# Kernel tuning notes

Measured on AMD Instinct MI355X. Metric: run time of the kernel, lower is better.

Reference implementation:

```python
import jax, jax.numpy as jnp
import numpy as np

B, S, EH, DH, A = 32, 2048, 512, 512, 512

def setup_inputs() -> dict:
    key = jax.random.key(0)
    k1, k2, k3, k4, k5 = jax.random.split(key, 5)
    decoder_hidden = jax.random.normal(k1, (2, B, DH), dtype=jnp.float32)
    encoder_outputs = jax.random.normal(k2, (B, S, 2 * EH), dtype=jnp.float32)
    # Linear weights stored as (in, out) for x @ W convention
    W = jax.random.normal(k3, (2 * EH, A), dtype=jnp.float32) / np.sqrt(2 * EH)
    U = jax.random.normal(k4, (2 * DH, A), dtype=jnp.float32) / np.sqrt(2 * DH)
    v = jax.random.normal(k5, (A, 1), dtype=jnp.float32) / np.sqrt(A)
    return {"decoder_hidden": decoder_hidden, "encoder_outputs": encoder_outputs,
            "W": W, "U": U, "v": v}

def reference(decoder_hidden, encoder_outputs, W, U, v):
    # (2, B, DH) -> (B, 2*DH), matching transpose(0,1).reshape(B, -1)
    b = decoder_hidden.shape[1]
    dh = jnp.transpose(decoder_hidden, (1, 0, 2)).reshape(b, -1)
    temp1 = jnp.einsum('bse,ea->bsa', encoder_outputs, W)   # (B, S, A)
    temp2 = dh @ U                                          # (B, A) — computed once, broadcast over S
    score = jnp.squeeze(jnp.tanh(temp1 + temp2[:, None, :]) @ v, -1)  # (B, S)
    attention_weights = jax.nn.softmax(score, axis=-1)      # (B, S)
    context_vector = jnp.einsum('bs,bse->be', attention_weights, encoder_outputs)[:, None, :]  # (B,1,2EH)
    return context_vector, attention_weights
```

## Files before the change

### kernel.cpp

```cpp
#include <hip/hip_runtime.h>
#include <hip/hip_bf16.h>

#define Bb 32
#define Ss 2048
#define Kk 1024
#define Aa 512

#define BM 128
#define BK 64
#define NT (Kk / BK)
#define ABUF (BM * BK * 2)
#define BBUF (Aa * BK * 2)

typedef __bf16 bf16x8 __attribute__((ext_vector_type(8)));
typedef float f32x4 __attribute__((ext_vector_type(4)));

__device__ __forceinline__ unsigned short f2bf(float f) {
  unsigned u = __float_as_uint(f);
  u += 0x7FFFu + ((u >> 16) & 1u);
  return (unsigned short)(u >> 16);
}

__device__ __forceinline__ float tanh_fast(float x) {
  float e = __expf(2.f * x);
  return (e - 1.f) / (e + 1.f);
}

__device__ __forceinline__ void gll16(const void* g, void* l) {
  __builtin_amdgcn_global_load_lds(
      (const __attribute__((address_space(1))) unsigned int*)g,
      (__attribute__((address_space(3))) unsigned int*)l, 16, 0, 0);
}

__global__ __launch_bounds__(256) void prep_wt(const float* __restrict__ W,
                                               unsigned short* __restrict__ WtT) {
  const int idx = blockIdx.x * 256 + threadIdx.x;
  const int a = idx & 511;
  const int g = idx >> 9;
  const int k0 = g * 8;
  const int t = k0 >> 6, kin = k0 & 63;
  unsigned short u[8];
#pragma unroll
  for (int j = 0; j < 8; ++j) u[j] = f2bf(W[(size_t)(k0 + j) * Aa + a]);
  uint4 pk;
  pk.x = (unsigned)u[0] | ((unsigned)u[1] << 16);
  pk.y = (unsigned)u[2] | ((unsigned)u[3] << 16);
  pk.z = (unsigned)u[4] | ((unsigned)u[5] << 16);
  pk.w = (unsigned)u[6] | ((unsigned)u[7] << 16);
  const size_t byteoff = (size_t)t * 65536 + a * 128 + (((kin * 2) ^ ((a & 7) << 4)));
  *(uint4*)((char*)WtT + byteoff) = pk;
}

__global__ __launch_bounds__(256) void t2_partial(const float* __restrict__ dh,
                                                  const float* __restrict__ U,
                                                  float* __restrict__ part) {
  const int b = blockIdx.x, kc = blockIdx.y, t = threadIdx.x;
  __shared__ float sdh[128];
  if (t < 128) {
    int k = kc * 128 + t;
    sdh[t] = dh[(k >> 9) * (Bb * 512) + b * 512 + (k & 511)];
  }
  __syncthreads();
#pragma unroll
  for (int h = 0; h < 2; ++h) {
    const int a = h * 256 + t;
    float s = 0.f;
#pragma unroll 8
    for (int kk = 0; kk < 128; ++kk) s += sdh[kk] * U[(size_t)(kc * 128 + kk) * Aa + a];
    part[(size_t)(b * 8 + kc) * Aa + a] = s;
  }
}

__global__ __launch_bounds__(256) void t2_reduce(const float* __restrict__ part,
                                                 float* __restrict__ t2) {
  const int idx = blockIdx.x * 256 + threadIdx.x;
  const int b = idx >> 9, a = idx & 511;
  float s = 0.f;
#pragma unroll
  for (int kc = 0; kc < 8; ++kc) s += part[(size_t)(b * 8 + kc) * Aa + a];
  t2[idx] = s;
}

#define STEP(curA, curB, nxtA, nxtB, T)                                         \
  {                                                                             \
    const int tn = (T) + 1;                                                     \
    float4 av0, av1, av2, av3;                                                  \
    if (tn < NT) {                                                              \
      const float* eb = encBase + tn * BK;                                      \
      av0 = *(const float4*)(eb + (size_t)(a_r0)      * Kk + a_c);              \
      av1 = *(const float4*)(eb + (size_t)(a_r0 + 32) * Kk + a_c);              \
      av2 = *(const float4*)(eb + (size_t)(a_r0 + 64) * Kk + a_c);              \
      av3 = *(const float4*)(eb + (size_t)(a_r0 + 96) * Kk + a_c);              \
      const char* gB = (const char*)WtT + (size_t)tn * 65536;                   \
      _Pragma("unroll")                                                         \
      for (int q = 0; q < 8; ++q)                                               \
        gll16(gB + (tid + q * 512) * 16, (nxtB) + (tid + q * 512) * 16);        \
    }                                                                           \
    _Pragma("unroll")                                                           \
    for (int kk = 0; kk < 2; ++kk) {                                            \
      bf16x8 af[4], bfr[8];                                                     \
      const int kb = (kk * 32 + ((lane >> 4) << 3)) * 2;                        \
      _Pragma("unroll")                                                         \
      for (int mi = 0; mi < 4; ++mi) {                                          \
        int r = wy * 64 + mi * 16 + (lane & 15);                                \
        af[mi] = *(const bf16x8*)((curA) + r * 128 + (kb ^ ((r & 7) << 4)));    \
      }                                                                         \
      _Pragma("unroll")                                                         \
      for (int ni = 0; ni < 8; ++ni) {                                          \
        int a = wx * 128 + ni * 16 + (lane & 15);                               \
        bfr[ni] = *(const bf16x8*)((curB) + a * 128 + (kb ^ ((a & 7) << 4)));   \
      }                                                                         \
      _Pragma("unroll")                                                         \
      for (int mi = 0; mi < 4; ++mi)                                            \
        _Pragma("unroll")                                                       \
        for (int ni = 0; ni < 8; ++ni)                                          \
          acc[mi][ni] = __builtin_amdgcn_mfma_f32_16x16x32_bf16(af[mi], bfr[ni], acc[mi][ni], 0, 0, 0); \
    }                                                                           \
    if (tn < NT) {                                                              \
      ushort4 w;                                                                \
      w.x = f2bf(av0.x); w.y = f2bf(av0.y); w.z = f2bf(av0.z); w.w = f2bf(av0.w); \
      *(ushort4*)((nxtA) + (a_r0)      * 128 + a_swz) = w;                      \
      w.x = f2bf(av1.x); w.y = f2bf(av1.y); w.z = f2bf(av1.z); w.w = f2bf(av1.w); \
      *(ushort4*)((nxtA) + (a_r0 + 32) * 128 + a_swz) = w;                      \
      w.x = f2bf(av2.x); w.y = f2bf(av2.y); w.z = f2bf(av2.z); w.w = f2bf(av2.w); \
      *(ushort4*)((nxtA) + (a_r0 + 64) * 128 + a_swz) = w;                      \
      w.x = f2bf(av3.x); w.y = f2bf(av3.y); w.z = f2bf(av3.z); w.w = f2bf(av3.w); \
      *(ushort4*)((nxtA) + (a_r0 + 96) * 128 + a_swz) = w;                      \
    }                                                                           \
    __syncthreads();                                                            \
  }

__global__ __launch_bounds__(512, 2) void score_gemm(const float* __restrict__ enc,
                                                     const unsigned short* __restrict__ WtT,
                                                     const float* __restrict__ t2,
                                                     const float* __restrict__ v,
                                                     float* __restrict__ score) {
  __shared__ __align__(16) char lds[2 * (ABUF + BBUF)];
  char* sA0 = lds;
  char* sA1 = lds + ABUF;
  char* sB0 = lds + 2 * ABUF;
  char* sB1 = lds + 2 * ABUF + BBUF;

  const int blk = blockIdx.x;
  const int b = blk >> 4, sc = blk & 15;
  const float* encBase = enc + (size_t)(b * Ss + sc * BM) * Kk;

  const int tid = threadIdx.x;
  const int lane = tid & 63;
  const int wid = tid >> 6;
  const int wy = wid >> 2, wx = wid & 3;

  const int a_r0 = tid >> 4;
  const int a_c = (tid & 15) << 2;
  const int a_swz = (a_c * 2) ^ ((a_r0 & 7) << 4);

  const f32x4 zero = {0.f, 0.f, 0.f, 0.f};
  f32x4 acc[4][8];
#pragma unroll
  for (int i = 0; i < 4; ++i)
#pragma unroll
    for (int j = 0; j < 8; ++j) acc[i][j] = zero;

  {
    float4 av0 = *(const float4*)(encBase + (size_t)(a_r0)      * Kk + a_c);
    float4 av1 = *(const float4*)(encBase + (size_t)(a_r0 + 32) * Kk + a_c);
    float4 av2 = *(const float4*)(encBase + (size_t)(a_r0 + 64) * Kk + a_c);
    float4 av3 = *(const float4*)(encBase + (size_t)(a_r0 + 96) * Kk + a_c);
#pragma unroll
    for (int q = 0; q < 8; ++q)
      gll16((const char*)WtT + (tid + q * 512) * 16, sB0 + (tid + q * 512) * 16);
    ushort4 w;
    w.x = f2bf(av0.x); w.y = f2bf(av0.y); w.z = f2bf(av0.z); w.w = f2bf(av0.w);
    *(ushort4*)(sA0 + (a_r0)      * 128 + a_swz) = w;
    w.x = f2bf(av1.x); w.y = f2bf(av1.y); w.z = f2bf(av1.z); w.w = f2bf(av1.w);
    *(ushort4*)(sA0 + (a_r0 + 32) * 128 + a_swz) = w;
    w.x = f2bf(av2.x); w.y = f2bf(av2.y); w.z = f2bf(av2.z); w.w = f2bf(av2.w);
    *(ushort4*)(sA0 + (a_r0 + 64) * 128 + a_swz) = w;
    w.x = f2bf(av3.x); w.y = f2bf(av3.y); w.z = f2bf(av3.z); w.w = f2bf(av3.w);
    *(ushort4*)(sA0 + (a_r0 + 96) * 128 + a_swz) = w;
    __syncthreads();
  }

  for (int t = 0; t < NT; t += 2) {
    STEP(sA0, sB0, sA1, sB1, t)
    STEP(sA1, sB1, sA0, sB0, t + 1)
  }

  float t2v[8], vv[8];
#pragma unroll
  for (int ni = 0; ni < 8; ++ni) {
    int c = wx * 128 + ni * 16 + (lane & 15);
    t2v[ni] = t2[b * Aa + c];
    vv[ni] = v[c];
  }
  float sp[4][4];
#pragma unroll
  for (int mi = 0; mi < 4; ++mi)
#pragma unroll
    for (int j = 0; j < 4; ++j) sp[mi][j] = 0.f;
#pragma unroll
  for (int mi = 0; mi < 4; ++mi)
#pragma unroll
    for (int ni = 0; ni < 8; ++ni)
#pragma unroll
      for (int j = 0; j < 4; ++j) {
        float x = acc[mi][ni][j] + t2v[ni];
        sp[mi][j] += vv[ni] * tanh_fast(x);
      }

  float* sbuf = (float*)lds;
#pragma unroll
  for (int mi = 0; mi < 4; ++mi)
#pragma unroll
    for (int j = 0; j < 4; ++j) {
      float s = sp[mi][j];
      s += __shfl_xor(s, 1);
      s += __shfl_xor(s, 2);
      s += __shfl_xor(s, 4);
      s += __shfl_xor(s, 8);
      if ((lane & 15) == 0) {
        int r = wy * 64 + mi * 16 + ((lane >> 4) << 2) + j;
        sbuf[r * 4 + wx] = s;
      }
    }
  __syncthreads();
  if (tid < BM) {
    float s = sbuf[tid * 4] + sbuf[tid * 4 + 1] + sbuf[tid * 4 + 2] + sbuf[tid * 4 + 3];
    score[b * Ss + sc * BM + tid] = s;
  }
}

__global__ __launch_bounds__(256) void softmax_k(float* __restrict__ aw) {
  const int b = blockIdx.x, t = threadIdx.x;
  __shared__ float red[8];
  float s[8];
  float m = -3.4e38f;
#pragma unroll
  for (int i = 0; i < 8; ++i) {
    s[i] = aw[b * Ss + t + i * 256];
    m = fmaxf(m, s[i]);
  }
#pragma unroll
  for (int off = 1; off < 64; off <<= 1) m = fmaxf(m, __shfl_xor(m, off));
  const int lane = t & 63, wv = t >> 6;
  if (lane == 0) red[wv] = m;
  __syncthreads();
  m = fmaxf(fmaxf(red[0], red[1]), fmaxf(red[2], red[3]));
  float e[8];
  float l = 0.f;
#pragma unroll
  for (int i = 0; i < 8; ++i) { e[i] = __expf(s[i] - m); l += e[i]; }
#pragma unroll
  for (int off = 1; off < 64; off <<= 1) l += __shfl_xor(l, off);
  if (lane == 0) red[4 + wv] = l;
  __syncthreads();
  l = red[4] + red[5] + red[6] + red[7];
  const float inv = 1.f / l;
#pragma unroll
  for (int i = 0; i < 8; ++i) aw[b * Ss + t + i * 256] = e[i] * inv;
}

__global__ __launch_bounds__(256) void ctx_partial(const float* __restrict__ enc,
                                                   const float* __restrict__ aw,
                                                   float* __restrict__ part) {
  const int b = blockIdx.x, ch = blockIdx.y, t = threadIdx.x;
  __shared__ float sw[64];
  const int s0 = ch * 64;
  if (t < 64) sw[t] = aw[b * Ss + s0 + t];
  __syncthreads();
  float ax = 0.f, ay = 0.f, az = 0.f, aww = 0.f;
  const float* ebase = enc + (size_t)(b * Ss + s0) * Kk + t * 4;
#pragma unroll 4
  for (int r = 0; r < 64; ++r) {
    const float4 ev = *(const float4*)(ebase + (size_t)r * Kk);
    const float w = sw[r];
    ax += w * ev.x; ay += w * ev.y; az += w * ev.z; aww += w * ev.w;
  }
  float4 o; o.x = ax; o.y = ay; o.z = az; o.w = aww;
  *(float4*)(part + (size_t)(b * 32 + ch) * Kk + t * 4) = o;
}

__global__ __launch_bounds__(256) void ctx_reduce(const float* __restrict__ part,
                                                  float* __restrict__ ctx) {
  const int idx = blockIdx.x * 256 + threadIdx.x;
  const int b = idx >> 10, e = idx & 1023;
  float s = 0.f;
#pragma unroll
  for (int ch = 0; ch < 32; ++ch) s += part[(size_t)(b * 32 + ch) * Kk + e];
  ctx[idx] = s;
}

extern "C" void kernel_launch(void* const* d_in, const int* in_sizes, int n_in,
                              void* d_out, int out_size, void* d_ws, size_t ws_size,
                              hipStream_t stream) {
  const float* dh  = (const float*)d_in[0];
  const float* enc = (const float*)d_in[1];
  const float* W   = (const float*)d_in[2];
  const float* U   = (const float*)d_in[3];
  const float* v   = (const float*)d_in[4];

  float* out_ctx = (float*)d_out;
  float* out_aw  = (float*)d_out + 32768;

  char* ws = (char*)d_ws;
  unsigned short* WtT = (unsigned short*)ws;
  float* t2p   = (float*)(ws + 1048576);
  float* t2    = (float*)(ws + 1048576 + 524288);
  float* cpart = (float*)(ws + 1048576 + 524288 + 65536);

  prep_wt<<<256, 256, 0, stream>>>(W, WtT);
  t2_partial<<<dim3(32, 8), 256, 0, stream>>>(dh, U, t2p);
  t2_reduce<<<64, 256, 0, stream>>>(t2p, t2);
  score_gemm<<<512, 512, 0, stream>>>(enc, WtT, t2, v, out_aw);
  softmax_k<<<32, 256, 0, stream>>>(out_aw);
  ctx_partial<<<dim3(32, 32), 256, 0, stream>>>(enc, out_aw, cpart);
  ctx_reduce<<<128, 256, 0, stream>>>(cpart, out_ctx);
}
```

Before: 196.8 us.

## Load fp32 encoder tiles directly to LDS and convert to bf16 at fragment read

The encoder A tile is now staged into LDS as raw fp32 with global_load_lds (direct-to-LDS DMA) and converted to bf16 only when fragments are read, instead of going through registers with a conversion and ds_write. The K step shrinks to 32, W's pre-transposed layout becomes a plain per-K-group layout, and the loop becomes a two-stage async pipeline with explicit vmcnt waits, raw s_barrier and setprio around the MFMA block. The aim is to take register staging and conversion off the load path and overlap global loads with compute. In exchange the A buffer needs twice the LDS per K element, conversion work is repeated by each wave reading the tile, and the occupancy hint of 2 blocks per CU is dropped.

```diff
diff --git a/kernel.cpp b/kernel.cpp
--- a/kernel.cpp
+++ b/kernel.cpp
@@ -7,13 +7,14 @@
 #define Aa 512
 
 #define BM 128
-#define BK 64
+#define BK 32
 #define NT (Kk / BK)
-#define ABUF (BM * BK * 2)
+#define ABUF (BM * BK * 4)
 #define BBUF (Aa * BK * 2)
 
 typedef __bf16 bf16x8 __attribute__((ext_vector_type(8)));
 typedef float f32x4 __attribute__((ext_vector_type(4)));
+typedef float f32x8 __attribute__((ext_vector_type(8)));
 
 __device__ __forceinline__ unsigned short f2bf(float f) {
   unsigned u = __float_as_uint(f);
@@ -36,9 +37,9 @@
                                                unsigned short* __restrict__ WtT) {
   const int idx = blockIdx.x * 256 + threadIdx.x;
   const int a = idx & 511;
-  const int g = idx >> 9;
-  const int k0 = g * 8;
-  const int t = k0 >> 6, kin = k0 & 63;
+  const int o = idx >> 9;
+  const int t = o >> 2, g = o & 3;
+  const int k0 = o * 8;
   unsigned short u[8];
 #pragma unroll
   for (int j = 0; j < 8; ++j) u[j] = f2bf(W[(size_t)(k0 + j) * Aa + a]);
@@ -47,8 +48,7 @@
   pk.y = (unsigned)u[2] | ((unsigned)u[3] << 16);
   pk.z = (unsigned)u[4] | ((unsigned)u[5] << 16);
   pk.w = (unsigned)u[6] | ((unsigned)u[7] << 16);
-  const size_t byteoff = (size_t)t * 65536 + a * 128 + (((kin * 2) ^ ((a & 7) << 4)));
-  *(uint4*)((char*)WtT + byteoff) = pk;
+  *(uint4*)((char*)WtT + (size_t)t * 32768 + g * 8192 + a * 16) = pk;
 }
 
 __global__ __launch_bounds__(256) void t2_partial(const float* __restrict__ dh,
@@ -81,60 +81,56 @@
   t2[idx] = s;
 }
 
-#define STEP(curA, curB, nxtA, nxtB, T)                                         \
+#define ITER(curA, curB, T)                                                     \
   {                                                                             \
-    const int tn = (T) + 1;                                                     \
-    float4 av0, av1, av2, av3;                                                  \
-    if (tn < NT) {                                                              \
-      const float* eb = encBase + tn * BK;                                      \
-      av0 = *(const float4*)(eb + (size_t)(a_r0)      * Kk + a_c);              \
-      av1 = *(const float4*)(eb + (size_t)(a_r0 + 32) * Kk + a_c);              \
-      av2 = *(const float4*)(eb + (size_t)(a_r0 + 64) * Kk + a_c);              \
-      av3 = *(const float4*)(eb + (size_t)(a_r0 + 96) * Kk + a_c);              \
-      const char* gB = (const char*)WtT + (size_t)tn * 65536;                   \
-      _Pragma("unroll")                                                         \
-      for (int q = 0; q < 8; ++q)                                               \
-        gll16(gB + (tid + q * 512) * 16, (nxtB) + (tid + q * 512) * 16);        \
+    bf16x8 af[4], bfr[8];                                                       \
+    _Pragma("unroll")                                                           \
+    for (int mi = 0; mi < 4; ++mi) {                                            \
+      const int r = wy * 64 + mi * 16 + (lane & 15);                            \
+      const int c0 = r * 8 + (((lane >> 4) * 2) ^ ((r & 3) << 1));              \
+      f32x4 lo = *(const f32x4*)((curA) + c0 * 16);                             \
+      f32x4 hi = *(const f32x4*)((curA) + c0 * 16 + 16);                        \
+      f32x8 w8 = {lo.x, lo.y, lo.z, lo.w, hi.x, hi.y, hi.z, hi.w};              \
+      af[mi] = __builtin_convertvector(w8, bf16x8);                             \
     }                                                                           \
     _Pragma("unroll")                                                           \
-    for (int kk = 0; kk < 2; ++kk) {                                            \
-      bf16x8 af[4], bfr[8];                                                     \
-      const int kb = (kk * 32 + ((lane >> 4) << 3)) * 2;                        \
+    for (int ni = 0; ni < 8; ++ni) {                                            \
+      const int a = wx * 128 + ni * 16 + (lane & 15);                           \
+      bfr[ni] = *(const bf16x8*)((curB) + (lane >> 4) * 8192 + a * 16);         \
+    }                                                                           \
+    __builtin_amdgcn_s_setprio(1);                                              \
+    _Pragma("unroll")                                                           \
+    for (int mi = 0; mi < 4; ++mi)                                              \
       _Pragma("unroll")                                                         \
-      for (int mi = 0; mi < 4; ++mi) {                                          \
-        int r = wy * 64 + mi * 16 + (lane & 15);                                \
-        af[mi] = *(const bf16x8*)((curA) + r * 128 + (kb ^ ((r & 7) << 4)));    \
-      }                                                                         \
-      _Pragma("unroll")                                                         \
-      for (int ni = 0; ni < 8; ++ni) {                                          \
-        int a = wx * 128 + ni * 16 + (lane & 15);                               \
-        bfr[ni] = *(const bf16x8*)((curB) + a * 128 + (kb ^ ((a & 7) << 4)));   \
-      }                                                                         \
-      _Pragma("unroll")                                                         \
-      for (int mi = 0; mi < 4; ++mi)                                            \
-        _Pragma("unroll")                                                       \
-        for (int ni = 0; ni < 8; ++ni)                                          \
-          acc[mi][ni] = __builtin_amdgcn_mfma_f32_16x16x32_bf16(af[mi], bfr[ni], acc[mi][ni], 0, 0, 0); \
+      for (int ni = 0; ni < 8; ++ni)                                            \
+        acc[mi][ni] = __builtin_amdgcn_mfma_f32_16x16x32_bf16(af[mi], bfr[ni], acc[mi][ni], 0, 0, 0); \
+    __builtin_amdgcn_s_setprio(0);                                              \
+    __builtin_amdgcn_sched_barrier(0);                                          \
+    __builtin_amdgcn_s_barrier();          \
+    if ((T) + 2 < NT) {                                                         \
+      const char* eb = encB + ((T) + 2) * 128;                                  \
+      gll16(eb + a_goff0, (curA) + a_loff0);                                    \
+      gll16(eb + a_goff1, (curA) + a_loff1);                                    \
+      const char* wb = wtB + (size_t)((T) + 2) * 32768;                         \
+      gll16(wb + b_off0, (curB) + b_off0);                                      \
+      gll16(wb + b_off1, (curB) + b_off1);                                      \
+      gll16(wb + b_off2, (curB) + b_off2);                                      \
+      gll16(wb + b_off3, (curB) + b_off3);                                      \
     }                                                                           \
-    if (tn < NT) {                                                              \
-      ushort4 w;                                                                \
-      w.x = f2bf(av0.x); w.y = f2bf(av0.y); w.z = f2bf(av0.z); w.w = f2bf(av0.w); \
-      *(ushort4*)((nxtA) + (a_r0)      * 128 + a_swz) = w;                      \
-      w.x = f2bf(av1.x); w.y = f2bf(av1.y); w.z = f2bf(av1.z); w.w = f2bf(av1.w); \
-      *(ushort4*)((nxtA) + (a_r0 + 32) * 128 + a_swz) = w;                      \
-      w.x = f2bf(av2.x); w.y = f2bf(av2.y); w.z = f2bf(av2.z); w.w = f2bf(av2.w); \
-      *(ushort4*)((nxtA) + (a_r0 + 64) * 128 + a_swz) = w;                      \
-      w.x = f2bf(av3.x); w.y = f2bf(av3.y); w.z = f2bf(av3.z); w.w = f2bf(av3.w); \
-      *(ushort4*)((nxtA) + (a_r0 + 96) * 128 + a_swz) = w;                      \
+    if ((T) < NT - 2) {                                                         \
+      asm volatile("s_waitcnt vmcnt(6)" ::: "memory");                          \
+    } else {                                                                    \
+      asm volatile("s_waitcnt vmcnt(0)" ::: "memory");                          \
     }                                                                           \
-    __syncthreads();                                                            \
-  }
-
-__global__ __launch_bounds__(512, 2) void score_gemm(const float* __restrict__ enc,
-                                                     const unsigned short* __restrict__ WtT,
-                                                     const float* __restrict__ t2,
-                                                     const float* __restrict__ v,
-                                                     float* __restrict__ score) {
+    __builtin_amdgcn_sched_barrier(0);                                          \
+    __builtin_amdgcn_s_barrier();                         \
+  }
+
+__global__ __launch_bounds__(512) void score_gemm(const float* __restrict__ enc,
+                                                  const unsigned short* __restrict__ WtT,
+                                                  const float* __restrict__ t2,
+                                                  const float* __restrict__ v,
+                                                  float* __restrict__ score) {
   __shared__ __align__(16) char lds[2 * (ABUF + BBUF)];
   char* sA0 = lds;
   char* sA1 = lds + ABUF;
@@ -143,16 +139,26 @@
 
   const int blk = blockIdx.x;
   const int b = blk >> 4, sc = blk & 15;
-  const float* encBase = enc + (size_t)(b * Ss + sc * BM) * Kk;
+  const char* encB = (const char*)(enc + (size_t)(b * Ss + sc * BM) * Kk);
+  const char* wtB = (const char*)WtT;
 
   const int tid = threadIdx.x;
   const int lane = tid & 63;
   const int wid = tid >> 6;
   const int wy = wid >> 2, wx = wid & 3;
 
-  const int a_r0 = tid >> 4;
-  const int a_c = (tid & 15) << 2;
-  const int a_swz = (a_c * 2) ^ ((a_r0 & 7) << 4);
+  const int a_c0 = tid, a_c1 = 512 + tid;
+  const int a_r0 = a_c0 >> 3, a_r1 = a_c1 >> 3;
+  const int a_h0 = (a_c0 & 7) ^ ((a_r0 & 3) << 1);
+  const int a_h1 = (a_c1 & 7) ^ ((a_r1 & 3) << 1);
+  const int a_goff0 = a_r0 * 4096 + a_h0 * 16;
+  const int a_goff1 = a_r1 * 4096 + a_h1 * 16;
+  const int a_loff0 = a_c0 * 16;
+  const int a_loff1 = a_c1 * 16;
+  const int b_off0 = tid * 16;
+  const int b_off1 = (512 + tid) * 16;
+  const int b_off2 = (1024 + tid) * 16;
+  const int b_off3 = (1536 + tid) * 16;
 
   const f32x4 zero = {0.f, 0.f, 0.f, 0.f};
   f32x4 acc[4][8];
@@ -162,28 +168,28 @@
     for (int j = 0; j < 8; ++j) acc[i][j] = zero;
 
   {
-    float4 av0 = *(const float4*)(encBase + (size_t)(a_r0)      * Kk + a_c);
-    float4 av1 = *(const float4*)(encBase + (size_t)(a_r0 + 32) * Kk + a_c);
-    float4 av2 = *(const float4*)(encBase + (size_t)(a_r0 + 64) * Kk + a_c);
-    float4 av3 = *(const float4*)(encBase + (size_t)(a_r0 + 96) * Kk + a_c);
-#pragma unroll
-    for (int q = 0; q < 8; ++q)
-      gll16((const char*)WtT + (tid + q * 512) * 16, sB0 + (tid + q * 512) * 16);
-    ushort4 w;
-    w.x = f2bf(av0.x); w.y = f2bf(av0.y); w.z = f2bf(av0.z); w.w = f2bf(av0.w);
-    *(ushort4*)(sA0 + (a_r0)      * 128 + a_swz) = w;
-    w.x = f2bf(av1.x); w.y = f2bf(av1.y); w.z = f2bf(av1.z); w.w = f2bf(av1.w);
-    *(ushort4*)(sA0 + (a_r0 + 32) * 128 + a_swz) = w;
-    w.x = f2bf(av2.x); w.y = f2bf(av2.y); w.z = f2bf(av2.z); w.w = f2bf(av2.w);
-    *(ushort4*)(sA0 + (a_r0 + 64) * 128 + a_swz) = w;
-    w.x = f2bf(av3.x); w.y = f2bf(av3.y); w.z = f2bf(av3.z); w.w = f2bf(av3.w);
-    *(ushort4*)(sA0 + (a_r0 + 96) * 128 + a_swz) = w;
-    __syncthreads();
+    gll16(encB + a_goff0, sA0 + a_loff0);
+    gll16(encB + a_goff1, sA0 + a_loff1);
+    gll16(wtB + b_off0, sB0 + b_off0);
+    gll16(wtB + b_off1, sB0 + b_off1);
+    gll16(wtB + b_off2, sB0 + b_off2);
+    gll16(wtB + b_off3, sB0 + b_off3);
+    const char* eb1 = encB + 128;
+    gll16(eb1 + a_goff0, sA1 + a_loff0);
+    gll16(eb1 + a_goff1, sA1 + a_loff1);
+    const char* wb1 = wtB + 32768;
+    gll16(wb1 + b_off0, sB1 + b_off0);
+    gll16(wb1 + b_off1, sB1 + b_off1);
+    gll16(wb1 + b_off2, sB1 + b_off2);
+    gll16(wb1 + b_off3, sB1 + b_off3);
+    asm volatile("s_waitcnt vmcnt(6)" ::: "memory");
+    __builtin_amdgcn_sched_barrier(0);
+    __builtin_amdgcn_s_barrier();
   }
 
   for (int t = 0; t < NT; t += 2) {
-    STEP(sA0, sB0, sA1, sB1, t)
-    STEP(sA1, sB1, sA0, sB0, t + 1)
+    ITER(sA0, sB0, t)
+    ITER(sA1, sB1, t + 1)
   }
 
   float t2v[8], vv[8];
```

Result: faster. 173.2 us (-12.0%).
